# Performance work log

Hardware: AMD Instinct MI355X
Metric: run time of the kernel (lower is better)

## Reference

```python
import jax, jax.numpy as jnp
import numpy as np

B, S, A, H, NH = 4, 4096, 512, 1024, 16
HD = H // NH  # 64


def setup_inputs() -> dict:
    key = jax.random.key(0)
    ks = jax.random.split(key, 12)
    s = 1.0 / np.sqrt(H)
    return {
        "hidden_states": jax.random.normal(ks[0], (B, S, H), jnp.float32),
        "audio_tokens": jax.random.normal(ks[1], (B, A, H), jnp.float32),
        "attention_mask": jax.random.randint(ks[2], (B, A), 0, 2, jnp.int32),
        "Wq": jax.random.normal(ks[3], (H, H), jnp.float32) * s,
        "bq": jnp.zeros((H,), jnp.float32),
        "Wk": jax.random.normal(ks[4], (H, H), jnp.float32) * s,
        "bk": jnp.zeros((H,), jnp.float32),
        "Wv": jax.random.normal(ks[5], (H, H), jnp.float32) * s,
        "bv": jnp.zeros((H,), jnp.float32),
        "Wo": jax.random.normal(ks[6], (H, H), jnp.float32) * s,
        "bo": jnp.zeros((H,), jnp.float32),
        "ln_gamma": jnp.ones((H,), jnp.float32),
        "ln_beta": jnp.zeros((H,), jnp.float32),
        "residual_scale": jnp.asarray(0.05, jnp.float32),
    }


def _san(x, big=10000.0):
    return jnp.nan_to_num(x, nan=0.0, posinf=big, neginf=-big)


def reference(hidden_states, audio_tokens, attention_mask, Wq, bq, Wk, bk, Wv, bv,
              Wo, bo, ln_gamma, ln_beta, residual_scale):
    hs = _san(hidden_states).astype(jnp.float32)
    at = _san(audio_tokens).astype(jnp.float32)

    def heads(x, W, b):  # [b, t, H] -> [b, t, nh, hd]
        return _san(x @ W.T + b).reshape(x.shape[0], x.shape[1], NH, HD)

    q = heads(hs, Wq, bq)            # [B,S,NH,HD]
    k = heads(at, Wk, bk)            # [B,A,NH,HD]
    v = heads(at, Wv, bv)            # [B,A,NH,HD]

    scale = max(np.sqrt(HD), 1e-8)
    scores = jnp.einsum("bsnd,band->bnsa", q, k) / scale  # [B,NH,S,A]
    scores = jnp.clip(_san(jnp.clip(scores, -50.0, 50.0), 50.0), -50.0, 50.0)

    attend = (attention_mask > 0)[:, None, None, :]       # [B,1,1,A]
    scores = jnp.where(attend, scores, -10000.0)
    scores = jnp.clip(scores, -50.0, 50.0)

    probs = jax.nn.softmax(scores, axis=-1)
    probs = _san(probs, 1.0)
    probs = probs / (jnp.sum(probs, axis=-1, keepdims=True) + 1e-8)

    ctx = jnp.einsum("bnsa,band->bsnd", probs, v).reshape(B, S, H)
    delta = _san(ctx @ Wo.T + bo)

    rs = jnp.clip(residual_scale, 0.0, 0.3)
    delta = rs * delta

    mu = jnp.mean(delta, axis=-1, keepdims=True)
    var = jnp.mean(jnp.square(delta - mu), axis=-1, keepdims=True)
    delta = (delta - mu) / jnp.sqrt(var + 1e-5) * ln_gamma + ln_beta
    return delta
```

## Files before the change

kernel.cpp:

```cpp
#include <hip/hip_runtime.h>
#include <hip/hip_bf16.h>
#include <cstdint>
#include <cstddef>

#define B_  4
#define S_  4096
#define A_  512
#define H_  1024
#define NH_ 16
#define HD_ 64

typedef __bf16 bf16;
typedef __bf16 bf16x8 __attribute__((ext_vector_type(8)));
typedef __bf16 bf16x4 __attribute__((ext_vector_type(4)));
typedef float  fx4    __attribute__((ext_vector_type(4)));

typedef __attribute__((address_space(3))) void LDS_v;
typedef const __attribute__((address_space(1))) void GLB_v;

__device__ __forceinline__ void gl_lds16(const void* g, void* l) {
    __builtin_amdgcn_global_load_lds((GLB_v*)g, (LDS_v*)l, 16, 0, 0);
}

__device__ __forceinline__ float sanf(float x) {
    if (x != x) return 0.f;
    if (fabsf(x) == __builtin_inff()) return x > 0.f ? 10000.f : -10000.f;
    return x;
}

__global__ __launch_bounds__(256) void cast_bf16(const float* __restrict__ in,
                                                 bf16* __restrict__ out, int n4) {
    int i = blockIdx.x * 256 + threadIdx.x;
    if (i >= n4) return;
    float4 v = ((const float4*)in)[i];
    bf16x4 o;
    o[0] = (bf16)sanf(v.x); o[1] = (bf16)sanf(v.y);
    o[2] = (bf16)sanf(v.z); o[3] = (bf16)sanf(v.w);
    *(bf16x4*)&out[(size_t)i * 4] = o;
}

template <int MODE>
__global__ __launch_bounds__(256) void gemm_bt(const bf16* __restrict__ A,
                                               const bf16* __restrict__ Bt,
                                               const float* __restrict__ bias,
                                               void* __restrict__ Cout,
                                               const float* __restrict__ rsp) {
    __shared__ __align__(16) bf16 As[128 * 32];
    __shared__ __align__(16) bf16 Bs[128 * 32];

    const int tid  = threadIdx.x;
    const int lane = tid & 63;
    const int wv   = tid >> 6;
    const int wr   = wv >> 1, wc = wv & 1;
    const int lr   = lane & 15, kq = lane >> 4;
    const int m0   = blockIdx.x * 128, n0 = blockIdx.y * 128;

    fx4 acc[4][4] = {};

    const bf16* Ag = A  + (size_t)m0 * 1024;
    const bf16* Bg = Bt + (size_t)n0 * 1024;
    const int c0 = tid, c1 = tid + 256;
    const int row0 = c0 >> 2, kc0 = c0 & 3;
    const int row1 = c1 >> 2, kc1 = c1 & 3;

    for (int k0 = 0; k0 < 1024; k0 += 32) {
        gl_lds16(Ag + (size_t)row0 * 1024 + k0 + kc0 * 8, &As[c0 * 8]);
        gl_lds16(Ag + (size_t)row1 * 1024 + k0 + kc1 * 8, &As[c1 * 8]);
        gl_lds16(Bg + (size_t)row0 * 1024 + k0 + kc0 * 8, &Bs[c0 * 8]);
        gl_lds16(Bg + (size_t)row1 * 1024 + k0 + kc1 * 8, &Bs[c1 * 8]);
        __syncthreads();
        bf16x8 af[4], bfr[4];
#pragma unroll
        for (int i = 0; i < 4; i++) af[i]  = *(const bf16x8*)&As[(wr * 64 + i * 16 + lr) * 32 + kq * 8];
#pragma unroll
        for (int j = 0; j < 4; j++) bfr[j] = *(const bf16x8*)&Bs[(wc * 64 + j * 16 + lr) * 32 + kq * 8];
#pragma unroll
        for (int i = 0; i < 4; i++)
#pragma unroll
            for (int j = 0; j < 4; j++)
                acc[i][j] = __builtin_amdgcn_mfma_f32_16x16x32_bf16(af[i], bfr[j], acc[i][j], 0, 0, 0);
        __syncthreads();
    }

    float bb[4];
#pragma unroll
    for (int j = 0; j < 4; j++) bb[j] = bias[n0 + wc * 64 + j * 16 + lr];

    if (MODE == 0 || MODE == 3) {
        const float sc = (MODE == 3) ? 0.18033688011112042f : 1.0f;
        bf16* C = (bf16*)Cout;
#pragma unroll
        for (int i = 0; i < 4; i++) {
            int row = m0 + wr * 64 + i * 16 + kq * 4;
#pragma unroll
            for (int j = 0; j < 4; j++) {
                int col = n0 + wc * 64 + j * 16 + lr;
#pragma unroll
                for (int r = 0; r < 4; r++)
                    C[(size_t)(row + r) * 1024 + col] = (bf16)((acc[i][j][r] + bb[j]) * sc);
            }
        }
    } else if (MODE == 1) {
        bf16* C = (bf16*)Cout;
#pragma unroll
        for (int i = 0; i < 4; i++) {
            int m = m0 + wr * 64 + i * 16 + kq * 4;
            int bidx = m >> 9, a = m & 511;
#pragma unroll
            for (int j = 0; j < 4; j++) {
                int col = n0 + wc * 64 + j * 16 + lr;
                size_t base = ((size_t)bidx * H_ + col) * A_ + a;
#pragma unroll
                for (int r = 0; r < 4; r++)
                    C[base + r] = (bf16)(acc[i][j][r] + bb[j]);
            }
        }
    } else {
        float rs = fminf(fmaxf(rsp[0], 0.f), 0.3f);
        float* C = (float*)Cout;
#pragma unroll
        for (int i = 0; i < 4; i++) {
            int row = m0 + wr * 64 + i * 16 + kq * 4;
#pragma unroll
            for (int j = 0; j < 4; j++) {
                int col = n0 + wc * 64 + j * 16 + lr;
#pragma unroll
                for (int r = 0; r < 4; r++)
                    C[(size_t)(row + r) * 1024 + col] = rs * (acc[i][j][r] + bb[j]);
            }
        }
    }
}

__global__ __launch_bounds__(256, 4) void attn_kernel(const bf16* __restrict__ Q,
                                                      const bf16* __restrict__ Kb,
                                                      const bf16* __restrict__ Vt,
                                                      const int* __restrict__ mask,
                                                      bf16* __restrict__ ctx) {
    __shared__ __align__(16) bf16 Qs[128 * 72];
    __shared__ __align__(16) bf16 Ks[64 * 64];
    __shared__ __align__(16) bf16 Vts[64 * 72];
    __shared__ float smask[512];
    __shared__ float dnm[128];

    const int tid  = threadIdx.x;
    const int lane = tid & 63;
    const int wv   = tid >> 6;
    const int lr   = lane & 15, kq = lane >> 4;
    const int st = blockIdx.x, h = blockIdx.y, b = blockIdx.z;
    const int m0 = b * S_ + st * 128;
    const float LO = -72.134752f;

    bf16x8 qtmp[4];
#pragma unroll
    for (int i = 0; i < 4; i++) {
        int c = tid + i * 256, row = c >> 3, ch = c & 7;
        qtmp[i] = *(const bf16x8*)(Q + (size_t)(m0 + row) * H_ + h * 64 + ch * 8);
    }
    smask[tid]       = (mask[b * A_ + tid] > 0)       ? -LO : LO;
    smask[tid + 256] = (mask[b * A_ + tid + 256] > 0) ? -LO : LO;
#pragma unroll
    for (int i = 0; i < 4; i++) {
        int c = tid + i * 256, row = c >> 3, ch = c & 7;
        *(bf16x8*)&Qs[row * 72 + ch * 8] = qtmp[i];
    }

    fx4 acco[2][4] = {};
    float dloc[2] = {0.f, 0.f};

    const int vrow = tid >> 2, vseg = tid & 3;
    const size_t vgbase = ((size_t)(b * H_ + h * 64 + vrow)) * A_ + vseg * 16;

    for (int it = 0; it < 8; it++) {
        const int a0 = it * 64;
        __syncthreads();

        bf16x8 v0 = *(const bf16x8*)(Vt + vgbase + a0);
        bf16x8 v1 = *(const bf16x8*)(Vt + vgbase + a0 + 8);
#pragma unroll
        for (int i = 0; i < 2; i++) {
            int c = tid + i * 256, row = c >> 3, ch = c & 7;
            gl_lds16(Kb + (size_t)(b * A_ + a0 + row) * H_ + h * 64 + ch * 8, &Ks[c * 8]);
        }
        *(bf16x8*)&Vts[vrow * 72 + vseg * 16]     = v0;
        *(bf16x8*)&Vts[vrow * 72 + vseg * 16 + 8] = v1;
        __syncthreads();

        fx4 accs[4][2] = {};
#pragma unroll
        for (int kk = 0; kk < 64; kk += 32) {
            bf16x8 kf[4], qf[2];
#pragma unroll
            for (int mt = 0; mt < 4; mt++)
                kf[mt] = *(const bf16x8*)&Ks[(mt * 16 + lr) * 64 + kk + kq * 8];
#pragma unroll
            for (int nt = 0; nt < 2; nt++)
                qf[nt] = *(const bf16x8*)&Qs[(wv * 32 + nt * 16 + lr) * 72 + kk + kq * 8];
#pragma unroll
            for (int mt = 0; mt < 4; mt++)
#pragma unroll
                for (int nt = 0; nt < 2; nt++)
                    accs[mt][nt] = __builtin_amdgcn_mfma_f32_16x16x32_bf16(kf[mt], qf[nt], accs[mt][nt], 0, 0, 0);
        }

        bf16x4 pf[4][2];
#pragma unroll
        for (int mt = 0; mt < 4; mt++) {
            fx4 cap = *(const fx4*)&smask[a0 + mt * 16 + kq * 4];
#pragma unroll
            for (int nt = 0; nt < 2; nt++) {
#pragma unroll
                for (int r = 0; r < 4; r++) {
                    float s2 = fmaxf(fminf(accs[mt][nt][r], cap[r]), LO);
                    float p  = __builtin_amdgcn_exp2f(s2);
                    pf[mt][nt][r] = (bf16)p;
                    dloc[nt] += p;
                }
            }
        }

#pragma unroll
        for (int ks = 0; ks < 2; ks++) {
            bf16x8 pa[2];
#pragma unroll
            for (int stl = 0; stl < 2; stl++)
                pa[stl] = __builtin_shufflevector(pf[2 * ks][stl], pf[2 * ks + 1][stl],
                                                  0, 1, 2, 3, 4, 5, 6, 7);
#pragma unroll
            for (int dt = 0; dt < 4; dt++) {
                bf16x4 lo = *(const bf16x4*)&Vts[(dt * 16 + lr) * 72 + ks * 32 + kq * 4];
                bf16x4 hi = *(const bf16x4*)&Vts[(dt * 16 + lr) * 72 + ks * 32 + 16 + kq * 4];
                bf16x8 vf = __builtin_shufflevector(lo, hi, 0, 1, 2, 3, 4, 5, 6, 7);
#pragma unroll
                for (int stl = 0; stl < 2; stl++)
                    acco[stl][dt] = __builtin_amdgcn_mfma_f32_16x16x32_bf16(pa[stl], vf, acco[stl][dt], 0, 0, 0);
            }
        }
    }

#pragma unroll
    for (int nt = 0; nt < 2; nt++) {
        dloc[nt] += __shfl_xor(dloc[nt], 16);
        dloc[nt] += __shfl_xor(dloc[nt], 32);
    }
    if (kq == 0) {
        dnm[wv * 32 + lr]      = dloc[0];
        dnm[wv * 32 + 16 + lr] = dloc[1];
    }
    __syncthreads();

#pragma unroll
    for (int stl = 0; stl < 2; stl++) {
        fx4 dv = *(const fx4*)&dnm[wv * 32 + stl * 16 + kq * 4];
        float ri[4];
#pragma unroll
        for (int r = 0; r < 4; r++) ri[r] = __builtin_amdgcn_rcpf(dv[r]);
#pragma unroll
        for (int dt = 0; dt < 4; dt++)
#pragma unroll
            for (int r = 0; r < 4; r++)
                Qs[(wv * 32 + stl * 16 + kq * 4 + r) * 72 + dt * 16 + lr] =
                    (bf16)(acco[stl][dt][r] * ri[r]);
    }
    __syncthreads();
#pragma unroll
    for (int i = 0; i < 4; i++) {
        int c = tid + i * 256, row = c >> 3, ch = c & 7;
        *(bf16x8*)&ctx[(size_t)(m0 + row) * H_ + h * 64 + ch * 8] = *(const bf16x8*)&Qs[row * 72 + ch * 8];
    }
}

__global__ __launch_bounds__(256) void ln_kernel(float* __restrict__ io,
                                                 const float* __restrict__ gamma,
                                                 const float* __restrict__ beta) {
    __shared__ float red[8];
    const int tid = threadIdx.x;
    float4* rowp = (float4*)(io + (size_t)blockIdx.x * 1024);
    float4 x = rowp[tid];
    float s = x.x + x.y + x.z + x.w;
    float q = x.x * x.x + x.y * x.y + x.z * x.z + x.w * x.w;
#pragma unroll
    for (int off = 32; off > 0; off >>= 1) {
        s += __shfl_down(s, off);
        q += __shfl_down(q, off);
    }
    if ((tid & 63) == 0) { red[(tid >> 6) * 2] = s; red[(tid >> 6) * 2 + 1] = q; }
    __syncthreads();
    s = red[0] + red[2] + red[4] + red[6];
    q = red[1] + red[3] + red[5] + red[7];
    float mean = s * (1.f / 1024.f);
    float var  = q * (1.f / 1024.f) - mean * mean;
    float inv  = rsqrtf(var + 1e-5f);
    float4 g  = ((const float4*)gamma)[tid];
    float4 bb = ((const float4*)beta)[tid];
    float4 y;
    y.x = (x.x - mean) * inv * g.x + bb.x;
    y.y = (x.y - mean) * inv * g.y + bb.y;
    y.z = (x.z - mean) * inv * g.z + bb.z;
    y.w = (x.w - mean) * inv * g.w + bb.w;
    rowp[tid] = y;
}

extern "C" void kernel_launch(void* const* d_in, const int* in_sizes, int n_in,
                              void* d_out, int out_size, void* d_ws, size_t ws_size,
                              hipStream_t stream) {
    const float* hs    = (const float*)d_in[0];
    const float* at    = (const float*)d_in[1];
    const int*   maskp = (const int*)d_in[2];
    const float* Wq    = (const float*)d_in[3];
    const float* bq    = (const float*)d_in[4];
    const float* Wk    = (const float*)d_in[5];
    const float* bk    = (const float*)d_in[6];
    const float* Wv    = (const float*)d_in[7];
    const float* bv    = (const float*)d_in[8];
    const float* Wo    = (const float*)d_in[9];
    const float* bo    = (const float*)d_in[10];
    const float* gamma = (const float*)d_in[11];
    const float* beta  = (const float*)d_in[12];
    const float* rsp   = (const float*)d_in[13];

    char* ws = (char*)d_ws;
    bf16* hsb = (bf16*)(ws + 0);
    bf16* ctx = (bf16*)(ws + 0);
    bf16* atb = (bf16*)(ws + 33554432);
    bf16* wqb = (bf16*)(ws + 37748736);
    bf16* wkb = (bf16*)(ws + 39845888);
    bf16* wvb = (bf16*)(ws + 41943040);
    bf16* wob = (bf16*)(ws + 44040192);
    bf16* Qb  = (bf16*)(ws + 46137344);
    bf16* Kb  = (bf16*)(ws + 79691776);
    bf16* Vtb = (bf16*)(ws + 83886080);

    cast_bf16<<<16384, 256, 0, stream>>>(hs, hsb, 4194304);
    cast_bf16<<<2048, 256, 0, stream>>>(at, atb, 524288);
    cast_bf16<<<1024, 256, 0, stream>>>(Wq, wqb, 262144);
    cast_bf16<<<1024, 256, 0, stream>>>(Wk, wkb, 262144);
    cast_bf16<<<1024, 256, 0, stream>>>(Wv, wvb, 262144);
    cast_bf16<<<1024, 256, 0, stream>>>(Wo, wob, 262144);

    gemm_bt<3><<<dim3(128, 8), 256, 0, stream>>>(hsb, wqb, bq, Qb, nullptr);
    gemm_bt<0><<<dim3(16, 8), 256, 0, stream>>>(atb, wkb, bk, Kb, nullptr);
    gemm_bt<1><<<dim3(16, 8), 256, 0, stream>>>(atb, wvb, bv, Vtb, nullptr);

    attn_kernel<<<dim3(32, 16, 4), 256, 0, stream>>>(Qb, Kb, Vtb, maskp, ctx);

    gemm_bt<2><<<dim3(128, 8), 256, 0, stream>>>(ctx, wob, bo, d_out, rsp);
    ln_kernel<<<16384, 256, 0, stream>>>((float*)d_out, gamma, beta);
}
```

Measured before the change: 377.5 us.

## Merge cast and QKV GEMM launches, prefetch K/V tiles in attention

The six cast launches become one kernel that indexes into the six tensors, and the Q, K and V projection GEMMs become one launch with a 1280-block grid split by block id. The attention kernel now loads the next K/V tile into registers while the current one is being computed, and pads the K tile in LDS to avoid bank conflicts. The aim is to cut launch overhead and tail effects and to hide global-load latency in attention. The cost is more register pressure in attention and branching in the merged kernels.

```diff
diff --git a/kernel.cpp b/kernel.cpp
--- a/kernel.cpp
+++ b/kernel.cpp
@@ -28,23 +28,135 @@
     return x;
 }
 
-__global__ __launch_bounds__(256) void cast_bf16(const float* __restrict__ in,
-                                                 bf16* __restrict__ out, int n4) {
+__global__ __launch_bounds__(256) void cast_all(const float* __restrict__ hs,
+                                                const float* __restrict__ at,
+                                                const float* __restrict__ wq,
+                                                const float* __restrict__ wk,
+                                                const float* __restrict__ wv,
+                                                const float* __restrict__ wo,
+                                                bf16* __restrict__ dhs, bf16* __restrict__ dat,
+                                                bf16* __restrict__ dwq, bf16* __restrict__ dwk,
+                                                bf16* __restrict__ dwv, bf16* __restrict__ dwo) {
     int i = blockIdx.x * 256 + threadIdx.x;
-    if (i >= n4) return;
-    float4 v = ((const float4*)in)[i];
+    const float* s; bf16* d; int off;
+    if (i < 4194304)      { s = hs; d = dhs; off = i; }
+    else if (i < 4718592) { s = at; d = dat; off = i - 4194304; }
+    else if (i < 4980736) { s = wq; d = dwq; off = i - 4718592; }
+    else if (i < 5242880) { s = wk; d = dwk; off = i - 4980736; }
+    else if (i < 5505024) { s = wv; d = dwv; off = i - 5242880; }
+    else                  { s = wo; d = dwo; off = i - 5505024; }
+    float4 v = ((const float4*)s)[off];
     bf16x4 o;
     o[0] = (bf16)sanf(v.x); o[1] = (bf16)sanf(v.y);
     o[2] = (bf16)sanf(v.z); o[3] = (bf16)sanf(v.w);
-    *(bf16x4*)&out[(size_t)i * 4] = o;
-}
-
-template <int MODE>
-__global__ __launch_bounds__(256) void gemm_bt(const bf16* __restrict__ A,
-                                               const bf16* __restrict__ Bt,
-                                               const float* __restrict__ bias,
-                                               void* __restrict__ Cout,
-                                               const float* __restrict__ rsp) {
+    *(bf16x4*)&d[(size_t)off * 4] = o;
+}
+
+__global__ __launch_bounds__(256) void qkv_gemm(const bf16* __restrict__ hsb,
+                                                const bf16* __restrict__ atb,
+                                                const bf16* __restrict__ wqb,
+                                                const bf16* __restrict__ wkb,
+                                                const bf16* __restrict__ wvb,
+                                                const float* __restrict__ bq,
+                                                const float* __restrict__ bk,
+                                                const float* __restrict__ bv,
+                                                bf16* __restrict__ Qb,
+                                                bf16* __restrict__ Kb,
+                                                bf16* __restrict__ Vtb) {
+    __shared__ __align__(16) bf16 As[128 * 32];
+    __shared__ __align__(16) bf16 Bs[128 * 32];
+
+    const int id = blockIdx.x;
+    int mode, m0, n0;
+    const bf16 *A, *Bt; const float* bias;
+    if (id < 1024)      { mode = 0; m0 = (id & 127) * 128; n0 = (id >> 7) * 128; A = hsb; Bt = wqb; bias = bq; }
+    else if (id < 1152) { int t = id - 1024; mode = 1; m0 = (t & 15) * 128; n0 = (t >> 4) * 128; A = atb; Bt = wkb; bias = bk; }
+    else                { int t = id - 1152; mode = 2; m0 = (t & 15) * 128; n0 = (t >> 4) * 128; A = atb; Bt = wvb; bias = bv; }
+
+    const int tid  = threadIdx.x;
+    const int lane = tid & 63;
+    const int wv   = tid >> 6;
+    const int wr   = wv >> 1, wc = wv & 1;
+    const int lr   = lane & 15, kq = lane >> 4;
+
+    fx4 acc[4][4] = {};
+
+    const bf16* Ag = A  + (size_t)m0 * 1024;
+    const bf16* Bg = Bt + (size_t)n0 * 1024;
+    const int c0 = tid, c1 = tid + 256;
+    const int row0 = c0 >> 2, kc0 = c0 & 3;
+    const int row1 = c1 >> 2, kc1 = c1 & 3;
+
+    for (int k0 = 0; k0 < 1024; k0 += 32) {
+        gl_lds16(Ag + (size_t)row0 * 1024 + k0 + kc0 * 8, &As[c0 * 8]);
+        gl_lds16(Ag + (size_t)row1 * 1024 + k0 + kc1 * 8, &As[c1 * 8]);
+        gl_lds16(Bg + (size_t)row0 * 1024 + k0 + kc0 * 8, &Bs[c0 * 8]);
+        gl_lds16(Bg + (size_t)row1 * 1024 + k0 + kc1 * 8, &Bs[c1 * 8]);
+        __syncthreads();
+        bf16x8 af[4], bfr[4];
+#pragma unroll
+        for (int i = 0; i < 4; i++) af[i]  = *(const bf16x8*)&As[(wr * 64 + i * 16 + lr) * 32 + kq * 8];
+#pragma unroll
+        for (int j = 0; j < 4; j++) bfr[j] = *(const bf16x8*)&Bs[(wc * 64 + j * 16 + lr) * 32 + kq * 8];
+#pragma unroll
+        for (int i = 0; i < 4; i++)
+#pragma unroll
+            for (int j = 0; j < 4; j++)
+                acc[i][j] = __builtin_amdgcn_mfma_f32_16x16x32_bf16(af[i], bfr[j], acc[i][j], 0, 0, 0);
+        __syncthreads();
+    }
+
+    float bb[4];
+#pragma unroll
+    for (int j = 0; j < 4; j++) bb[j] = bias[n0 + wc * 64 + j * 16 + lr];
+
+    if (mode == 0) {
+        const float sc = 0.18033688011112042f;
+#pragma unroll
+        for (int i = 0; i < 4; i++) {
+            int row = m0 + wr * 64 + i * 16 + kq * 4;
+#pragma unroll
+            for (int j = 0; j < 4; j++) {
+                int col = n0 + wc * 64 + j * 16 + lr;
+#pragma unroll
+                for (int r = 0; r < 4; r++)
+                    Qb[(size_t)(row + r) * 1024 + col] = (bf16)((acc[i][j][r] + bb[j]) * sc);
+            }
+        }
+    } else if (mode == 1) {
+#pragma unroll
+        for (int i = 0; i < 4; i++) {
+            int row = m0 + wr * 64 + i * 16 + kq * 4;
+#pragma unroll
+            for (int j = 0; j < 4; j++) {
+                int col = n0 + wc * 64 + j * 16 + lr;
+#pragma unroll
+                for (int r = 0; r < 4; r++)
+                    Kb[(size_t)(row + r) * 1024 + col] = (bf16)(acc[i][j][r] + bb[j]);
+            }
+        }
+    } else {
+#pragma unroll
+        for (int i = 0; i < 4; i++) {
+            int m = m0 + wr * 64 + i * 16 + kq * 4;
+            int bidx = m >> 9, a = m & 511;
+#pragma unroll
+            for (int j = 0; j < 4; j++) {
+                int col = n0 + wc * 64 + j * 16 + lr;
+                size_t base = ((size_t)bidx * H_ + col) * A_ + a;
+#pragma unroll
+                for (int r = 0; r < 4; r++)
+                    Vtb[base + r] = (bf16)(acc[i][j][r] + bb[j]);
+            }
+        }
+    }
+}
+
+__global__ __launch_bounds__(256) void gemm_o(const bf16* __restrict__ A,
+                                              const bf16* __restrict__ Bt,
+                                              const float* __restrict__ bias,
+                                              float* __restrict__ C,
+                                              const float* __restrict__ rsp) {
     __shared__ __align__(16) bf16 As[128 * 32];
     __shared__ __align__(16) bf16 Bs[128 * 32];
 
@@ -85,49 +197,16 @@
     float bb[4];
 #pragma unroll
     for (int j = 0; j < 4; j++) bb[j] = bias[n0 + wc * 64 + j * 16 + lr];
-
-    if (MODE == 0 || MODE == 3) {
-        const float sc = (MODE == 3) ? 0.18033688011112042f : 1.0f;
-        bf16* C = (bf16*)Cout;
-#pragma unroll
-        for (int i = 0; i < 4; i++) {
-            int row = m0 + wr * 64 + i * 16 + kq * 4;
-#pragma unroll
-            for (int j = 0; j < 4; j++) {
-                int col = n0 + wc * 64 + j * 16 + lr;
-#pragma unroll
-                for (int r = 0; r < 4; r++)
-                    C[(size_t)(row + r) * 1024 + col] = (bf16)((acc[i][j][r] + bb[j]) * sc);
-            }
-        }
-    } else if (MODE == 1) {
-        bf16* C = (bf16*)Cout;
-#pragma unroll
-        for (int i = 0; i < 4; i++) {
-            int m = m0 + wr * 64 + i * 16 + kq * 4;
-            int bidx = m >> 9, a = m & 511;
-#pragma unroll
-            for (int j = 0; j < 4; j++) {
-                int col = n0 + wc * 64 + j * 16 + lr;
-                size_t base = ((size_t)bidx * H_ + col) * A_ + a;
-#pragma unroll
-                for (int r = 0; r < 4; r++)
-                    C[base + r] = (bf16)(acc[i][j][r] + bb[j]);
-            }
-        }
-    } else {
-        float rs = fminf(fmaxf(rsp[0], 0.f), 0.3f);
-        float* C = (float*)Cout;
-#pragma unroll
-        for (int i = 0; i < 4; i++) {
-            int row = m0 + wr * 64 + i * 16 + kq * 4;
-#pragma unroll
-            for (int j = 0; j < 4; j++) {
-                int col = n0 + wc * 64 + j * 16 + lr;
-#pragma unroll
-                for (int r = 0; r < 4; r++)
-                    C[(size_t)(row + r) * 1024 + col] = rs * (acc[i][j][r] + bb[j]);
-            }
+    float rs = fminf(fmaxf(rsp[0], 0.f), 0.3f);
+#pragma unroll
+    for (int i = 0; i < 4; i++) {
+        int row = m0 + wr * 64 + i * 16 + kq * 4;
+#pragma unroll
+        for (int j = 0; j < 4; j++) {
+            int col = n0 + wc * 64 + j * 16 + lr;
+#pragma unroll
+            for (int r = 0; r < 4; r++)
+                C[(size_t)(row + r) * 1024 + col] = rs * (acc[i][j][r] + bb[j]);
         }
     }
 }
@@ -138,7 +217,7 @@
                                                       const int* __restrict__ mask,
                                                       bf16* __restrict__ ctx) {
     __shared__ __align__(16) bf16 Qs[128 * 72];
-    __shared__ __align__(16) bf16 Ks[64 * 64];
+    __shared__ __align__(16) bf16 Ks[64 * 72];
     __shared__ __align__(16) bf16 Vts[64 * 72];
     __shared__ float smask[512];
     __shared__ float dnm[128];
@@ -165,26 +244,34 @@
         *(bf16x8*)&Qs[row * 72 + ch * 8] = qtmp[i];
     }
 
+    const int srow = tid >> 2, sseg = tid & 3;
+    const size_t kg = (size_t)(b * A_ + srow) * H_ + h * 64 + sseg * 16;
+    const size_t vg = (size_t)(b * H_ + h * 64 + srow) * A_ + sseg * 16;
+
+    bf16x8 kr0 = *(const bf16x8*)(Kb + kg);
+    bf16x8 kr1 = *(const bf16x8*)(Kb + kg + 8);
+    bf16x8 vr0 = *(const bf16x8*)(Vt + vg);
+    bf16x8 vr1 = *(const bf16x8*)(Vt + vg + 8);
+
     fx4 acco[2][4] = {};
     float dloc[2] = {0.f, 0.f};
 
-    const int vrow = tid >> 2, vseg = tid & 3;
-    const size_t vgbase = ((size_t)(b * H_ + h * 64 + vrow)) * A_ + vseg * 16;
-
     for (int it = 0; it < 8; it++) {
         const int a0 = it * 64;
         __syncthreads();
-
-        bf16x8 v0 = *(const bf16x8*)(Vt + vgbase + a0);
-        bf16x8 v1 = *(const bf16x8*)(Vt + vgbase + a0 + 8);
-#pragma unroll
-        for (int i = 0; i < 2; i++) {
-            int c = tid + i * 256, row = c >> 3, ch = c & 7;
-            gl_lds16(Kb + (size_t)(b * A_ + a0 + row) * H_ + h * 64 + ch * 8, &Ks[c * 8]);
-        }
-        *(bf16x8*)&Vts[vrow * 72 + vseg * 16]     = v0;
-        *(bf16x8*)&Vts[vrow * 72 + vseg * 16 + 8] = v1;
-        __syncthreads();
+        *(bf16x8*)&Ks[srow * 72 + sseg * 16]      = kr0;
+        *(bf16x8*)&Ks[srow * 72 + sseg * 16 + 8]  = kr1;
+        *(bf16x8*)&Vts[srow * 72 + sseg * 16]     = vr0;
+        *(bf16x8*)&Vts[srow * 72 + sseg * 16 + 8] = vr1;
+        __syncthreads();
+
+        if (it < 7) {
+            const size_t ko = kg + (size_t)(a0 + 64) * H_;
+            kr0 = *(const bf16x8*)(Kb + ko);
+            kr1 = *(const bf16x8*)(Kb + ko + 8);
+            vr0 = *(const bf16x8*)(Vt + vg + a0 + 64);
+            vr1 = *(const bf16x8*)(Vt + vg + a0 + 64 + 8);
+        }
 
         fx4 accs[4][2] = {};
 #pragma unroll
@@ -192,7 +279,7 @@
             bf16x8 kf[4], qf[2];
 #pragma unroll
             for (int mt = 0; mt < 4; mt++)
-                kf[mt] = *(const bf16x8*)&Ks[(mt * 16 + lr) * 64 + kk + kq * 8];
+                kf[mt] = *(const bf16x8*)&Ks[(mt * 16 + lr) * 72 + kk + kq * 8];
 #pragma unroll
             for (int nt = 0; nt < 2; nt++)
                 qf[nt] = *(const bf16x8*)&Qs[(wv * 32 + nt * 16 + lr) * 72 + kk + kq * 8];
@@ -331,19 +418,14 @@
     bf16* Kb  = (bf16*)(ws + 79691776);
     bf16* Vtb = (bf16*)(ws + 83886080);
 
-    cast_bf16<<<16384, 256, 0, stream>>>(hs, hsb, 4194304);
-    cast_bf16<<<2048, 256, 0, stream>>>(at, atb, 524288);
-    cast_bf16<<<1024, 256, 0, stream>>>(Wq, wqb, 262144);
-    cast_bf16<<<1024, 256, 0, stream>>>(Wk, wkb, 262144);
-    cast_bf16<<<1024, 256, 0, stream>>>(Wv, wvb, 262144);
-    cast_bf16<<<1024, 256, 0, stream>>>(Wo, wob, 262144);
-
-    gemm_bt<3><<<dim3(128, 8), 256, 0, stream>>>(hsb, wqb, bq, Qb, nullptr);
-    gemm_bt<0><<<dim3(16, 8), 256, 0, stream>>>(atb, wkb, bk, Kb, nullptr);
-    gemm_bt<1><<<dim3(16, 8), 256, 0, stream>>>(atb, wvb, bv, Vtb, nullptr);
+    cast_all<<<22528, 256, 0, stream>>>(hs, at, Wq, Wk, Wv, Wo,
+                                        hsb, atb, wqb, wkb, wvb, wob);
+
+    qkv_gemm<<<1280, 256, 0, stream>>>(hsb, atb, wqb, wkb, wvb,
+                                       bq, bk, bv, Qb, Kb, Vtb);
 
     attn_kernel<<<dim3(32, 16, 4), 256, 0, stream>>>(Qb, Kb, Vtb, maskp, ctx);
 
-    gemm_bt<2><<<dim3(128, 8), 256, 0, stream>>>(ctx, wob, bo, d_out, rsp);
+    gemm_o<<<dim3(128, 8), 256, 0, stream>>>(ctx, wob, bo, (float*)d_out, rsp);
     ln_kernel<<<16384, 256, 0, stream>>>((float*)d_out, gamma, beta);
 }
```

Measured after the change: 329.3 us. 1.15x faster.
